# Optimization experiments

Hardware: AMD Instinct MI355X
Metric: run time of the kernel (lower is better)

Reference implementation:

```python
import jax, jax.numpy as jnp
import numpy as np

N_WIN = 7
NUM_HEADS = 8
DIM = 256
QK = 256
TOPK = 4
MLP_HID = 4 * DIM
SCALE = QK ** -0.5  # used for both region routing and pixel attention (qk_scale=None)


def _layernorm(x, g, b, eps=1e-6):
    mu = jnp.mean(x, axis=-1, keepdims=True)
    var = jnp.mean(jnp.square(x - mu), axis=-1, keepdims=True)
    return (x - mu) * jax.lax.rsqrt(var + eps) * g + b


def _dwconv(x, w, b):
    # x: NHWC, w: (5,5,1,C) depthwise kernel (torch Conv2d groups=C, padding=2)
    y = jax.lax.conv_general_dilated(
        x, w, window_strides=(1, 1), padding='SAME',
        feature_group_count=x.shape[-1],
        dimension_numbers=('NHWC', 'HWIO', 'NHWC'))
    return y + b


def _bra(x, qkv_w, qkv_b, lepe_w, lepe_b, wo_w, wo_b):
    # BiLevelRoutingAttention, NHWC in/out
    N, H, W, C = x.shape
    j = i = N_WIN
    h, w = H // j, W // i
    p2, w2, m = j * i, h * w, NUM_HEADS
    dq, dv = QK // m, C // m
    # window partition: (N, p2, h, w, C)
    xw = x.reshape(N, j, h, i, w, C).transpose(0, 1, 3, 2, 4, 5).reshape(N, p2, h, w, C)
    qkv = xw @ qkv_w + qkv_b
    q = qkv[..., :QK]            # (N,p2,h,w,QK)
    kv = qkv[..., QK:]           # (N,p2,h,w,QK+C)
    q_pix = q.reshape(N, p2, w2, QK)
    kv_pix = kv.reshape(N, p2, w2, QK + C)
    q_win = jnp.mean(q, axis=(2, 3))                    # (N,p2,QK)
    k_win = jnp.mean(kv[..., :QK], axis=(2, 3))         # (N,p2,QK)
    # LePE: depthwise conv on V in full-image layout
    v_img = kv[..., QK:].reshape(N, j, i, h, w, C).transpose(0, 1, 3, 2, 4, 5).reshape(N, H, W, C)
    lepe = _dwconv(v_img, lepe_w, lepe_b)
    # region-to-region routing, top-k window selection
    logit = jnp.einsum('npc,nqc->npq', q_win * SCALE, k_win)    # (N,p2,p2)
    _, r_idx = jax.lax.top_k(logit, TOPK)                       # (N,p2,TOPK)
    # gather KV of selected windows: (N,p2,TOPK,w2,QK+C)
    kv_sel = kv_pix[jnp.arange(N)[:, None, None], r_idx]
    k_sel = kv_sel[..., :QK].reshape(N, p2, TOPK * w2, m, dq).transpose(0, 1, 3, 2, 4)  # (N,p2,m,kw2,dq)
    v_sel = kv_sel[..., QK:].reshape(N, p2, TOPK * w2, m, dv).transpose(0, 1, 3, 2, 4)  # (N,p2,m,kw2,dv)
    q_h = q_pix.reshape(N, p2, w2, m, dq).transpose(0, 1, 3, 2, 4)                      # (N,p2,m,w2,dq)
    aw = jnp.einsum('npmqd,npmkd->npmqk', q_h * SCALE, k_sel)
    aw = jax.nn.softmax(aw, axis=-1)
    out = jnp.einsum('npmqk,npmkd->npmqd', aw, v_sel)           # (N,p2,m,w2,dv)
    out = out.transpose(0, 1, 3, 2, 4).reshape(N, j, i, h, w, C)
    out = out.transpose(0, 1, 3, 2, 4, 5).reshape(N, H, W, C)
    out = out + lepe
    return out @ wo_w + wo_b


def setup_inputs() -> dict:
    key = jax.random.key(0)
    ks = jax.random.split(key, 8)
    s = 0.02
    return {
        'x': jax.random.normal(ks[0], (8, 56, 56, DIM), dtype=jnp.float32),
        'ln1_g': jnp.ones((DIM,), jnp.float32),
        'ln1_b': jnp.zeros((DIM,), jnp.float32),
        'qkv_w': jax.random.normal(ks[1], (DIM, 2 * QK + DIM), jnp.float32) * s,
        'qkv_b': jnp.zeros((2 * QK + DIM,), jnp.float32),
        'lepe_w': jax.random.normal(ks[2], (5, 5, 1, DIM), jnp.float32) * s,
        'lepe_b': jnp.zeros((DIM,), jnp.float32),
        'wo_w': jax.random.normal(ks[3], (DIM, DIM), jnp.float32) * s,
        'wo_b': jnp.zeros((DIM,), jnp.float32),
        'ln2_g': jnp.ones((DIM,), jnp.float32),
        'ln2_b': jnp.zeros((DIM,), jnp.float32),
        'mlp_w1': jax.random.normal(ks[4], (DIM, MLP_HID), jnp.float32) * s,
        'mlp_b1': jnp.zeros((MLP_HID,), jnp.float32),
        'mlp_w2': jax.random.normal(ks[5], (MLP_HID, DIM), jnp.float32) * s,
        'mlp_b2': jnp.zeros((DIM,), jnp.float32),
    }


def reference(x, ln1_g, ln1_b, qkv_w, qkv_b, lepe_w, lepe_b, wo_w, wo_b,
              ln2_g, ln2_b, mlp_w1, mlp_b1, mlp_w2, mlp_b2):
    x = x + _bra(_layernorm(x, ln1_g, ln1_b), qkv_w, qkv_b, lepe_w, lepe_b, wo_w, wo_b)
    h = _layernorm(x, ln2_g, ln2_b)
    h = jax.nn.gelu(h @ mlp_w1 + mlp_b1, approximate=False) @ mlp_w2 + mlp_b2
    return x + h
```

## Files before the change

kernel.cpp:

```cpp
#include <hip/hip_runtime.h>
#include <hip/hip_bf16.h>

#define NIMG 8
#define HW 56
#define CDIM 256
#define TOK (NIMG*HW*HW)
#define NWIN 49
#define NPW (NIMG*NWIN)
#define ATT_SCALE 0.0625f

typedef __attribute__((ext_vector_type(8))) short short8;
typedef __attribute__((ext_vector_type(4))) short short4v;
typedef __attribute__((ext_vector_type(4))) float f32x4;

static const size_t OFF_WQKV  = 0;
static const size_t OFF_WWO   = 393216;
static const size_t OFF_W1    = 524288;
static const size_t OFF_W2    = 1048576;
static const size_t OFF_XLN   = 1572864;
static const size_t OFF_QKV   = 14417920;
static const size_t OFF_QKWIN = 52953088;
static const size_t OFF_RIDX  = 53755904;
static const size_t OFF_ATTN  = 53762176;
static const size_t OFF_HMID  = OFF_XLN;

__device__ __forceinline__ float gelu_exact(float v) {
    return 0.5f * v * (1.f + erff(v * 0.70710678118654752f));
}
__device__ __forceinline__ short f2bs(float x) {
    __hip_bfloat16 h = __float2bfloat16(x);
    return *(short*)&h;
}
__device__ __forceinline__ float bs2f(short s) {
    return __uint_as_float(((unsigned)(unsigned short)s) << 16);
}
__device__ __forceinline__ void gld16(const short* g, short* l) {
    __builtin_amdgcn_global_load_lds(
        (const __attribute__((address_space(1))) void*)g,
        (__attribute__((address_space(3))) void*)l, 16, 0, 0);
}

__global__ __launch_bounds__(256) void transpose_cast4_k(const float* __restrict__ s0,
                                                         const float* __restrict__ s1,
                                                         const float* __restrict__ s2,
                                                         const float* __restrict__ s3,
                                                         __hip_bfloat16* __restrict__ d0,
                                                         __hip_bfloat16* __restrict__ d1,
                                                         __hip_bfloat16* __restrict__ d2,
                                                         __hip_bfloat16* __restrict__ d3) {
    int b = blockIdx.x;
    const float* src; __hip_bfloat16* dst; int K, N, l;
    if (b < 192)      { src = s0; dst = d0; K = 256;  N = 768;  l = b; }
    else if (b < 256) { src = s1; dst = d1; K = 256;  N = 256;  l = b - 192; }
    else if (b < 512) { src = s2; dst = d2; K = 256;  N = 1024; l = b - 256; }
    else              { src = s3; dst = d3; K = 1024; N = 256;  l = b - 512; }
    int nx = N / 32;
    int n0 = (l % nx) * 32, k0 = (l / nx) * 32;
    __shared__ float t[32][33];
    int tx = threadIdx.x & 31, ty = threadIdx.x >> 5;
    #pragma unroll
    for (int i = 0; i < 32; i += 8)
        t[ty + i][tx] = src[(size_t)(k0 + ty + i) * N + n0 + tx];
    __syncthreads();
    #pragma unroll
    for (int i = 0; i < 32; i += 8)
        dst[(size_t)(n0 + ty + i) * K + k0 + tx] = __float2bfloat16(t[tx][ty + i]);
}

__global__ __launch_bounds__(256) void ln_bf_k(const float* __restrict__ in,
                                               const float* __restrict__ g,
                                               const float* __restrict__ b,
                                               short* __restrict__ out, int remap) {
    int t = blockIdx.x * 4 + (threadIdx.x >> 6);
    int lane = threadIdx.x & 63;
    float4 v = *(const float4*)(in + (size_t)t * 256 + lane * 4);
    float s = v.x + v.y + v.z + v.w;
    float s2 = v.x * v.x + v.y * v.y + v.z * v.z + v.w * v.w;
    #pragma unroll
    for (int o = 32; o > 0; o >>= 1) {
        s  += __shfl_xor(s, o);
        s2 += __shfl_xor(s2, o);
    }
    float mu = s * (1.f / 256.f);
    float rstd = rsqrtf(s2 * (1.f / 256.f) - mu * mu + 1e-6f);
    float4 gv = *(const float4*)(g + lane * 4);
    float4 bv = *(const float4*)(b + lane * 4);
    short4v o;
    o[0] = f2bs((v.x - mu) * rstd * gv.x + bv.x);
    o[1] = f2bs((v.y - mu) * rstd * gv.y + bv.y);
    o[2] = f2bs((v.z - mu) * rstd * gv.z + bv.z);
    o[3] = f2bs((v.w - mu) * rstd * gv.w + bv.w);
    size_t tb;
    if (remap) {
        int n = t / 3136, rem = t % 3136, y = rem / 56, x = rem % 56;
        int p = (y >> 3) * 7 + (x >> 3);
        int si = (y & 7) * 8 + (x & 7);
        tb = (size_t)(n * 49 + p) * 64 + si;
    } else {
        tb = (size_t)t;
    }
    *(short4v*)(out + tb * 256 + lane * 4) = o;
}

template<int MODE>
__global__ __launch_bounds__(256) void gemm97(const short* __restrict__ A,
                                              const short* __restrict__ Bt,
                                              const float* __restrict__ bias,
                                              const float* __restrict__ res, void* Cv,
                                              int M, int N, int K) {
    const int bn = blockIdx.x * 128;
    const int bm = blockIdx.y * 128;
    const int tid = threadIdx.x;
    const int wave = tid >> 6, lane = tid & 63;
    const int l15 = lane & 15, quad = lane >> 4;
    const int wm = (wave & 1) * 64, wn = (wave >> 1) * 64;

    __shared__ __align__(16) short smem[10240];
    short* As = smem;
    short* Bs = smem + 4096;

    f32x4 acc[4][4];
    #pragma unroll
    for (int i = 0; i < 4; ++i)
        #pragma unroll
        for (int j = 0; j < 4; ++j) acc[i][j] = (f32x4){0.f, 0.f, 0.f, 0.f};

    const int ca = wave * 2;
    const int crow = lane >> 2;
    const int ckq = (lane & 3) * 8;
    const short* ga0 = A  + (size_t)(bm + ca * 16 + crow) * K + ckq;
    const short* ga1 = ga0 + (size_t)16 * K;
    const short* gb0 = Bt + (size_t)(bn + ca * 16 + crow) * K + ckq;
    const short* gb1 = gb0 + (size_t)16 * K;
    short* la0 = As + ca * 512;
    short* lb0 = Bs + ca * 512;

    for (int k0 = 0; k0 < K; k0 += 32) {
        gld16(ga0 + k0, la0);
        gld16(ga1 + k0, la0 + 512);
        gld16(gb0 + k0, lb0);
        gld16(gb1 + k0, lb0 + 512);
        __syncthreads();
        short8 af[4], bfr[4];
        #pragma unroll
        for (int i = 0; i < 4; ++i)
            af[i] = *(const short8*)&As[(wm + i * 16 + l15) * 32 + quad * 8];
        #pragma unroll
        for (int j = 0; j < 4; ++j)
            bfr[j] = *(const short8*)&Bs[(wn + j * 16 + l15) * 32 + quad * 8];
        #pragma unroll
        for (int i = 0; i < 4; ++i)
            #pragma unroll
            for (int j = 0; j < 4; ++j)
                acc[i][j] = __builtin_amdgcn_mfma_f32_16x16x32_bf16(af[i], bfr[j], acc[i][j], 0, 0, 0);
        __syncthreads();
    }

    if (MODE == 1) {
        #pragma unroll
        for (int i = 0; i < 4; ++i) {
            int row = bm + wm + i * 16 + quad * 4;
            #pragma unroll
            for (int j = 0; j < 4; ++j) {
                int col = bn + wn + j * 16 + l15;
                float bia = bias[col];
                #pragma unroll
                for (int r = 0; r < 4; ++r) {
                    size_t idx = (size_t)(row + r) * N + col;
                    ((float*)Cv)[idx] = acc[i][j][r] + bia + res[idx];
                }
            }
        }
    } else {
        float biasv[4];
        #pragma unroll
        for (int j = 0; j < 4; ++j) biasv[j] = bias[bn + wn + j * 16 + l15];
        short* ep = &smem[wave * 2560];
        short* outp = (short*)Cv;
        #pragma unroll
        for (int p = 0; p < 2; ++p) {
            #pragma unroll
            for (int i = 0; i < 4; ++i)
                #pragma unroll
                for (int jj = 0; jj < 2; ++jj) {
                    int j = p * 2 + jj;
                    #pragma unroll
                    for (int r = 0; r < 4; ++r) {
                        float v = acc[i][j][r] + biasv[j];
                        if (MODE == 2) v = gelu_exact(v);
                        ep[(i * 16 + quad * 4 + r) * 40 + jj * 16 + l15] = f2bs(v);
                    }
                }
            __builtin_amdgcn_s_waitcnt(0);
            int c = lane & 3;
            #pragma unroll
            for (int rr = 0; rr < 4; ++rr) {
                int row = rr * 16 + (lane >> 2);
                short8 v = *(const short8*)&ep[row * 40 + c * 8];
                *(short8*)&outp[(size_t)(bm + wm + row) * N + bn + wn + p * 32 + c * 8] = v;
            }
            __builtin_amdgcn_s_waitcnt(0);
        }
    }
}

__global__ __launch_bounds__(256) void win_means_k(const short* __restrict__ qkv,
                                                   float* __restrict__ qkwin) {
    int w = blockIdx.x;
    int cg = (threadIdx.x & 63) * 8;
    int sp = threadIdx.x >> 6;
    float s[8] = {0.f, 0.f, 0.f, 0.f, 0.f, 0.f, 0.f, 0.f};
    const short* base = qkv + (size_t)w * 64 * 768 + cg;
    for (int si = sp; si < 64; si += 4) {
        short8 v = *(const short8*)(base + (size_t)si * 768);
        #pragma unroll
        for (int i = 0; i < 8; ++i) s[i] += bs2f(v[i]);
    }
    __shared__ float red[4][512];
    #pragma unroll
    for (int i = 0; i < 8; ++i) red[sp][cg + i] = s[i];
    __syncthreads();
    for (int c = threadIdx.x; c < 512; c += 256) {
        float t = red[0][c] + red[1][c] + red[2][c] + red[3][c];
        qkwin[(size_t)w * 512 + c] = t * (1.f / 64.f);
    }
}

__global__ __launch_bounds__(64) void route_k(const float* __restrict__ qkwin,
                                              int* __restrict__ ridx) {
    int w = blockIdx.x;
    int n = w / 49;
    int tid = threadIdx.x;
    __shared__ float qv[256];
    __shared__ float lg[49];
    for (int i = tid; i < 256; i += 64) qv[i] = qkwin[(size_t)w * 512 + i] * ATT_SCALE;
    __syncthreads();
    if (tid < 49) {
        const float* kp = qkwin + (size_t)(n * 49 + tid) * 512 + 256;
        float d = 0.f;
        for (int cc = 0; cc < 256; ++cc) d += qv[cc] * kp[cc];
        lg[tid] = d;
    }
    __syncthreads();
    if (tid == 0) {
        #pragma unroll
        for (int t = 0; t < 4; ++t) {
            float best = -1e30f; int bi = 0;
            for (int j = 0; j < 49; ++j)
                if (lg[j] > best) { best = lg[j]; bi = j; }
            lg[bi] = -1e30f;
            ridx[w * 4 + t] = bi;
        }
    }
}

__global__ __launch_bounds__(256) void attn_mfma_k(const short* __restrict__ qkv,
                                                   const int* __restrict__ ridx,
                                                   short* __restrict__ attn) {
    const int blk = blockIdx.x;
    const int w = blk >> 3, h = blk & 7;
    const int n = w / 49;
    const int tid = threadIdx.x;
    const int wave = tid >> 6, lane = tid & 63;
    const int l15 = lane & 15, quad = lane >> 4;

    __shared__ __align__(16) short Ks[256 * 40];
    __shared__ __align__(16) short Vt[32 * 264];
    __shared__ __align__(16) short Ps[4 * 16 * 264];
    __shared__ int rs4[4];
    if (tid < 4) rs4[tid] = ridx[w * 4 + tid];
    __syncthreads();

    {
        int s = tid >> 2, kq = (tid & 3) * 8;
        #pragma unroll
        for (int u = 0; u < 4; ++u) {
            int key = u * 64 + s;
            const short* src = qkv + ((size_t)(n * 49 + rs4[u]) * 64 + s) * 768 + 256 + h * 32 + kq;
            *(short8*)&Ks[key * 40 + kq] = *(const short8*)src;
        }
    }
    {
        int key = tid;
        int t = key >> 6, s = key & 63;
        const short* src = qkv + ((size_t)(n * 49 + rs4[t]) * 64 + s) * 768 + 512 + h * 32;
        #pragma unroll
        for (int u = 0; u < 4; ++u) {
            short8 v = *(const short8*)(src + u * 8);
            #pragma unroll
            for (int i = 0; i < 8; ++i)
                Vt[(u * 8 + i) * 264 + key] = v[i];
        }
    }
    __syncthreads();

    const short* qp = qkv + ((size_t)w * 64 + wave * 16 + l15) * 768 + h * 32 + quad * 8;
    short8 qf = *(const short8*)qp;

    f32x4 st[16];
    #pragma unroll
    for (int j = 0; j < 16; ++j) {
        short8 kf = *(const short8*)&Ks[(j * 16 + l15) * 40 + quad * 8];
        st[j] = __builtin_amdgcn_mfma_f32_16x16x32_bf16(qf, kf, (f32x4){0.f, 0.f, 0.f, 0.f}, 0, 0, 0);
    }

    float lr[4];
    short* pw = &Ps[wave * 16 * 264];
    #pragma unroll
    for (int r = 0; r < 4; ++r) {
        float mx = -1e30f;
        #pragma unroll
        for (int j = 0; j < 16; ++j) mx = fmaxf(mx, st[j][r]);
        #pragma unroll
        for (int off = 1; off < 16; off <<= 1) mx = fmaxf(mx, __shfl_xor(mx, off));
        float sum = 0.f;
        #pragma unroll
        for (int j = 0; j < 16; ++j) {
            float p = __expf((st[j][r] - mx) * ATT_SCALE);
            sum += p;
            pw[(quad * 4 + r) * 264 + j * 16 + l15] = f2bs(p);
        }
        #pragma unroll
        for (int off = 1; off < 16; off <<= 1) sum += __shfl_xor(sum, off);
        lr[r] = sum;
    }
    __syncthreads();

    f32x4 oc[2] = {(f32x4){0.f,0.f,0.f,0.f}, (f32x4){0.f,0.f,0.f,0.f}};
    #pragma unroll
    for (int kk = 0; kk < 8; ++kk) {
        short8 pf = *(const short8*)&pw[l15 * 264 + kk * 32 + quad * 8];
        #pragma unroll
        for (int jj = 0; jj < 2; ++jj) {
            short8 vf = *(const short8*)&Vt[(jj * 16 + l15) * 264 + kk * 32 + quad * 8];
            oc[jj] = __builtin_amdgcn_mfma_f32_16x16x32_bf16(pf, vf, oc[jj], 0, 0, 0);
        }
    }

    short* op = attn + ((size_t)w * 64 + wave * 16) * 256 + h * 32;
    #pragma unroll
    for (int jj = 0; jj < 2; ++jj)
        #pragma unroll
        for (int r = 0; r < 4; ++r)
            op[(size_t)(quad * 4 + r) * 256 + jj * 16 + l15] = f2bs(oc[jj][r] / lr[r]);
}

__global__ __launch_bounds__(256) void lepe_k(const short* __restrict__ qkv,
                                              const short* __restrict__ attn,
                                              const float* __restrict__ lw,
                                              const float* __restrict__ lb,
                                              short* __restrict__ ywo) {
    int t = blockIdx.x * 8 + (threadIdx.x >> 5);
    int c0 = (threadIdx.x & 31) * 8;
    int n = t / 3136, rem = t % 3136, y = rem / 56, x = rem % 56;
    float sum[8];
    {
        float4 b0 = *(const float4*)(lb + c0), b1 = *(const float4*)(lb + c0 + 4);
        sum[0] = b0.x; sum[1] = b0.y; sum[2] = b0.z; sum[3] = b0.w;
        sum[4] = b1.x; sum[5] = b1.y; sum[6] = b1.z; sum[7] = b1.w;
    }
    #pragma unroll
    for (int ky = 0; ky < 5; ++ky) {
        int yy = y + ky - 2;
        if ((unsigned)yy >= 56u) continue;
        #pragma unroll
        for (int kx = 0; kx < 5; ++kx) {
            int xx = x + kx - 2;
            if ((unsigned)xx >= 56u) continue;
            int p = (yy >> 3) * 7 + (xx >> 3);
            int si = (yy & 7) * 8 + (xx & 7);
            short8 v = *(const short8*)(qkv + ((size_t)(n * 49 + p) * 64 + si) * 768 + 512 + c0);
            const float* wp = lw + (ky * 5 + kx) * 256 + c0;
            float4 w0 = *(const float4*)wp, w1 = *(const float4*)(wp + 4);
            sum[0] += bs2f(v[0]) * w0.x; sum[1] += bs2f(v[1]) * w0.y;
            sum[2] += bs2f(v[2]) * w0.z; sum[3] += bs2f(v[3]) * w0.w;
            sum[4] += bs2f(v[4]) * w1.x; sum[5] += bs2f(v[5]) * w1.y;
            sum[6] += bs2f(v[6]) * w1.z; sum[7] += bs2f(v[7]) * w1.w;
        }
    }
    int p0 = (y >> 3) * 7 + (x >> 3);
    int s0 = (y & 7) * 8 + (x & 7);
    short8 a = *(const short8*)(attn + ((size_t)(n * 49 + p0) * 64 + s0) * 256 + c0);
    short8 o;
    #pragma unroll
    for (int i = 0; i < 8; ++i) o[i] = f2bs(sum[i] + bs2f(a[i]));
    *(short8*)(ywo + (size_t)t * 256 + c0) = o;
}

extern "C" void kernel_launch(void* const* d_in, const int* in_sizes, int n_in,
                              void* d_out, int out_size, void* d_ws, size_t ws_size,
                              hipStream_t stream) {
    const float* x      = (const float*)d_in[0];
    const float* ln1_g  = (const float*)d_in[1];
    const float* ln1_b  = (const float*)d_in[2];
    const float* qkv_w  = (const float*)d_in[3];
    const float* qkv_b  = (const float*)d_in[4];
    const float* lepe_w = (const float*)d_in[5];
    const float* lepe_b = (const float*)d_in[6];
    const float* wo_w   = (const float*)d_in[7];
    const float* wo_b   = (const float*)d_in[8];
    const float* ln2_g  = (const float*)d_in[9];
    const float* ln2_b  = (const float*)d_in[10];
    const float* mlp_w1 = (const float*)d_in[11];
    const float* mlp_b1 = (const float*)d_in[12];
    const float* mlp_w2 = (const float*)d_in[13];
    const float* mlp_b2 = (const float*)d_in[14];
    float* out = (float*)d_out;

    char* ws = (char*)d_ws;
    __hip_bfloat16* wqkvT = (__hip_bfloat16*)(ws + OFF_WQKV);
    __hip_bfloat16* wwoT  = (__hip_bfloat16*)(ws + OFF_WWO);
    __hip_bfloat16* w1T   = (__hip_bfloat16*)(ws + OFF_W1);
    __hip_bfloat16* w2T   = (__hip_bfloat16*)(ws + OFF_W2);
    short* xln   = (short*)(ws + OFF_XLN);
    short* qkvb  = (short*)(ws + OFF_QKV);
    float* qkwin = (float*)(ws + OFF_QKWIN);
    int*   ridx  = (int*)(ws + OFF_RIDX);
    short* attnb = (short*)(ws + OFF_ATTN);
    short* ywo   = (short*)(ws + OFF_XLN);
    short* h2    = (short*)(ws + OFF_ATTN);
    short* hmid  = (short*)(ws + OFF_HMID);

    transpose_cast4_k<<<768, 256, 0, stream>>>(qkv_w, wo_w, mlp_w1, mlp_w2,
                                               wqkvT, wwoT, w1T, w2T);
    ln_bf_k<<<TOK/4, 256, 0, stream>>>(x, ln1_g, ln1_b, xln, 1);
    gemm97<0><<<dim3(6, 196), 256, 0, stream>>>(xln, (const short*)wqkvT,
                                                qkv_b, nullptr, qkvb, TOK, 768, 256);
    win_means_k<<<NPW, 256, 0, stream>>>(qkvb, qkwin);
    route_k<<<NPW, 64, 0, stream>>>(qkwin, ridx);
    attn_mfma_k<<<NPW * 8, 256, 0, stream>>>(qkvb, ridx, attnb);
    lepe_k<<<TOK/8, 256, 0, stream>>>(qkvb, attnb, lepe_w, lepe_b, ywo);
    gemm97<1><<<dim3(2, 196), 256, 0, stream>>>(ywo, (const short*)wwoT,
                                                wo_b, x, out, TOK, 256, 256);
    ln_bf_k<<<TOK/4, 256, 0, stream>>>(out, ln2_g, ln2_b, h2, 0);
    gemm97<2><<<dim3(8, 196), 256, 0, stream>>>(h2, (const short*)w1T,
                                                mlp_b1, nullptr, hmid, TOK, 1024, 256);
    gemm97<1><<<dim3(2, 196), 256, 0, stream>>>(hmid, (const short*)w2T,
                                                mlp_b2, out, out, TOK, 256, 1024);
}
```

Baseline: 344.5 us.

## Fuse window-mean reduction into QKV GEMM epilogue and add smaller-tile residual GEMM

The QKV GEMM epilogue now reduces each 64-row wave tile (one window) per column and writes the q/k window means directly, which removes the separate win_means_k pass over the QKV buffer. The residual-output GEMMs (N=256) move to a new 64x128-tile kernel launched on twice as many blocks, to fill the GPU better on these narrow GEMMs. The tradeoff is that the window means are now computed from fp32 accumulators instead of bf16-rounded values, and the smaller tiles reuse less of each loaded B tile.

Result: faster. 318.8 us (-7.5%).

```diff
diff --git a/kernel.cpp b/kernel.cpp
--- a/kernel.cpp
+++ b/kernel.cpp
@@ -102,11 +102,11 @@
     *(short4v*)(out + tb * 256 + lane * 4) = o;
 }
 
-template<int MODE>
+template<int MODE, bool QMEANS>
 __global__ __launch_bounds__(256) void gemm97(const short* __restrict__ A,
                                               const short* __restrict__ Bt,
                                               const float* __restrict__ bias,
-                                              const float* __restrict__ res, void* Cv,
+                                              void* Cv, float* __restrict__ qkwin,
                                               int M, int N, int K) {
     const int bn = blockIdx.x * 128;
     const int bm = blockIdx.y * 128;
@@ -156,73 +156,120 @@
         __syncthreads();
     }
 
-    if (MODE == 1) {
-        #pragma unroll
-        for (int i = 0; i < 4; ++i) {
-            int row = bm + wm + i * 16 + quad * 4;
-            #pragma unroll
-            for (int j = 0; j < 4; ++j) {
-                int col = bn + wn + j * 16 + l15;
-                float bia = bias[col];
+    if (QMEANS && bn < 512) {
+        float s[4];
+        #pragma unroll
+        for (int j = 0; j < 4; ++j) {
+            float t = 0.f;
+            #pragma unroll
+            for (int i = 0; i < 4; ++i)
+                #pragma unroll
+                for (int r = 0; r < 4; ++r) t += acc[i][j][r];
+            t += __shfl_xor(t, 16);
+            t += __shfl_xor(t, 32);
+            s[j] = t;
+        }
+        float v = (quad == 0) ? s[0] : (quad == 1) ? s[1] : (quad == 2) ? s[2] : s[3];
+        int col = bn + wn + quad * 16 + l15;
+        int win = (bm + wm) >> 6;
+        qkwin[(size_t)win * 512 + col] = v * (1.f / 64.f) + bias[col];
+    }
+
+    float biasv[4];
+    #pragma unroll
+    for (int j = 0; j < 4; ++j) biasv[j] = bias[bn + wn + j * 16 + l15];
+    short* ep = &smem[wave * 2560];
+    short* outp = (short*)Cv;
+    #pragma unroll
+    for (int p = 0; p < 2; ++p) {
+        #pragma unroll
+        for (int i = 0; i < 4; ++i)
+            #pragma unroll
+            for (int jj = 0; jj < 2; ++jj) {
+                int j = p * 2 + jj;
                 #pragma unroll
                 for (int r = 0; r < 4; ++r) {
-                    size_t idx = (size_t)(row + r) * N + col;
-                    ((float*)Cv)[idx] = acc[i][j][r] + bia + res[idx];
+                    float v = acc[i][j][r] + biasv[j];
+                    if (MODE == 2) v = gelu_exact(v);
+                    ep[(i * 16 + quad * 4 + r) * 40 + jj * 16 + l15] = f2bs(v);
                 }
             }
-        }
-    } else {
-        float biasv[4];
-        #pragma unroll
-        for (int j = 0; j < 4; ++j) biasv[j] = bias[bn + wn + j * 16 + l15];
-        short* ep = &smem[wave * 2560];
-        short* outp = (short*)Cv;
-        #pragma unroll
-        for (int p = 0; p < 2; ++p) {
-            #pragma unroll
-            for (int i = 0; i < 4; ++i)
-                #pragma unroll
-                for (int jj = 0; jj < 2; ++jj) {
-                    int j = p * 2 + jj;
-                    #pragma unroll
-                    for (int r = 0; r < 4; ++r) {
-                        float v = acc[i][j][r] + biasv[j];
-                        if (MODE == 2) v = gelu_exact(v);
-                        ep[(i * 16 + quad * 4 + r) * 40 + jj * 16 + l15] = f2bs(v);
-                    }
-                }
-            __builtin_amdgcn_s_waitcnt(0);
-            int c = lane & 3;
-            #pragma unroll
-            for (int rr = 0; rr < 4; ++rr) {
-                int row = rr * 16 + (lane >> 2);
-                short8 v = *(const short8*)&ep[row * 40 + c * 8];
-                *(short8*)&outp[(size_t)(bm + wm + row) * N + bn + wn + p * 32 + c * 8] = v;
+        __builtin_amdgcn_s_waitcnt(0);
+        int c = lane & 3;
+        #pragma unroll
+        for (int rr = 0; rr < 4; ++rr) {
+            int row = rr * 16 + (lane >> 2);
+            short8 v = *(const short8*)&ep[row * 40 + c * 8];
+            *(short8*)&outp[(size_t)(bm + wm + row) * N + bn + wn + p * 32 + c * 8] = v;
+        }
+        __builtin_amdgcn_s_waitcnt(0);
+    }
+}
+
+__global__ __launch_bounds__(256) void gemm_s(const short* __restrict__ A,
+                                              const short* __restrict__ Bt,
+                                              const float* __restrict__ bias,
+                                              const float* __restrict__ res,
+                                              float* __restrict__ C,
+                                              int M, int N, int K) {
+    const int bn = blockIdx.x * 128;
+    const int bm = blockIdx.y * 64;
+    const int tid = threadIdx.x;
+    const int wave = tid >> 6, lane = tid & 63;
+    const int l15 = lane & 15, quad = lane >> 4;
+    const int wm = (wave & 1) * 32, wn = (wave >> 1) * 64;
+
+    __shared__ __align__(16) short As[64 * 32];
+    __shared__ __align__(16) short Bs[128 * 32];
+
+    f32x4 acc[2][4];
+    #pragma unroll
+    for (int i = 0; i < 2; ++i)
+        #pragma unroll
+        for (int j = 0; j < 4; ++j) acc[i][j] = (f32x4){0.f, 0.f, 0.f, 0.f};
+
+    const int crow = lane >> 2;
+    const int ckq = (lane & 3) * 8;
+    const short* ga  = A  + (size_t)(bm + wave * 16 + crow) * K + ckq;
+    const short* gb0 = Bt + (size_t)(bn + wave * 16 + crow) * K + ckq;
+    const short* gb1 = gb0 + (size_t)64 * K;
+    short* la  = As + wave * 512;
+    short* lb0 = Bs + wave * 512;
+    short* lb1 = Bs + 2048 + wave * 512;
+
+    for (int k0 = 0; k0 < K; k0 += 32) {
+        gld16(ga + k0, la);
+        gld16(gb0 + k0, lb0);
+        gld16(gb1 + k0, lb1);
+        __syncthreads();
+        short8 af[2], bfr[4];
+        #pragma unroll
+        for (int i = 0; i < 2; ++i)
+            af[i] = *(const short8*)&As[(wm + i * 16 + l15) * 32 + quad * 8];
+        #pragma unroll
+        for (int j = 0; j < 4; ++j)
+            bfr[j] = *(const short8*)&Bs[(wn + j * 16 + l15) * 32 + quad * 8];
+        #pragma unroll
+        for (int i = 0; i < 2; ++i)
+            #pragma unroll
+            for (int j = 0; j < 4; ++j)
+                acc[i][j] = __builtin_amdgcn_mfma_f32_16x16x32_bf16(af[i], bfr[j], acc[i][j], 0, 0, 0);
+        __syncthreads();
+    }
+
+    #pragma unroll
+    for (int i = 0; i < 2; ++i) {
+        int row = bm + wm + i * 16 + quad * 4;
+        #pragma unroll
+        for (int j = 0; j < 4; ++j) {
+            int col = bn + wn + j * 16 + l15;
+            float bia = bias[col];
+            #pragma unroll
+            for (int r = 0; r < 4; ++r) {
+                size_t idx = (size_t)(row + r) * N + col;
+                C[idx] = acc[i][j][r] + bia + res[idx];
             }
-            __builtin_amdgcn_s_waitcnt(0);
-        }
-    }
-}
-
-__global__ __launch_bounds__(256) void win_means_k(const short* __restrict__ qkv,
-                                                   float* __restrict__ qkwin) {
-    int w = blockIdx.x;
-    int cg = (threadIdx.x & 63) * 8;
-    int sp = threadIdx.x >> 6;
-    float s[8] = {0.f, 0.f, 0.f, 0.f, 0.f, 0.f, 0.f, 0.f};
-    const short* base = qkv + (size_t)w * 64 * 768 + cg;
-    for (int si = sp; si < 64; si += 4) {
-        short8 v = *(const short8*)(base + (size_t)si * 768);
-        #pragma unroll
-        for (int i = 0; i < 8; ++i) s[i] += bs2f(v[i]);
-    }
-    __shared__ float red[4][512];
-    #pragma unroll
-    for (int i = 0; i < 8; ++i) red[sp][cg + i] = s[i];
-    __syncthreads();
-    for (int c = threadIdx.x; c < 512; c += 256) {
-        float t = red[0][c] + red[1][c] + red[2][c] + red[3][c];
-        qkwin[(size_t)w * 512 + c] = t * (1.f / 64.f);
+        }
     }
 }
 
@@ -424,17 +471,16 @@
     transpose_cast4_k<<<768, 256, 0, stream>>>(qkv_w, wo_w, mlp_w1, mlp_w2,
                                                wqkvT, wwoT, w1T, w2T);
     ln_bf_k<<<TOK/4, 256, 0, stream>>>(x, ln1_g, ln1_b, xln, 1);
-    gemm97<0><<<dim3(6, 196), 256, 0, stream>>>(xln, (const short*)wqkvT,
-                                                qkv_b, nullptr, qkvb, TOK, 768, 256);
-    win_means_k<<<NPW, 256, 0, stream>>>(qkvb, qkwin);
+    gemm97<0, true><<<dim3(6, 196), 256, 0, stream>>>(xln, (const short*)wqkvT,
+                                                      qkv_b, qkvb, qkwin, TOK, 768, 256);
     route_k<<<NPW, 64, 0, stream>>>(qkwin, ridx);
     attn_mfma_k<<<NPW * 8, 256, 0, stream>>>(qkvb, ridx, attnb);
     lepe_k<<<TOK/8, 256, 0, stream>>>(qkvb, attnb, lepe_w, lepe_b, ywo);
-    gemm97<1><<<dim3(2, 196), 256, 0, stream>>>(ywo, (const short*)wwoT,
-                                                wo_b, x, out, TOK, 256, 256);
+    gemm_s<<<dim3(2, 392), 256, 0, stream>>>(ywo, (const short*)wwoT,
+                                             wo_b, x, out, TOK, 256, 256);
     ln_bf_k<<<TOK/4, 256, 0, stream>>>(out, ln2_g, ln2_b, h2, 0);
-    gemm97<2><<<dim3(8, 196), 256, 0, stream>>>(h2, (const short*)w1T,
-                                                mlp_b1, nullptr, hmid, TOK, 1024, 256);
-    gemm97<1><<<dim3(2, 196), 256, 0, stream>>>(hmid, (const short*)w2T,
-                                                mlp_b2, out, out, TOK, 256, 1024);
-}
+    gemm97<2, false><<<dim3(8, 196), 256, 0, stream>>>(h2, (const short*)w1T,
+                                                       mlp_b1, hmid, nullptr, TOK, 1024, 256);
+    gemm_s<<<dim3(2, 392), 256, 0, stream>>>(hmid, (const short*)w2T,
+                                             mlp_b2, out, out, TOK, 256, 1024);
+}
```
